# Optimization experiments

Hardware: AMD Instinct MI355X
Metric: run time of the kernel (lower is better)

Reference implementation:

```python
import jax, jax.numpy as jnp
import numpy as np

N_HEAD = 12

def setup_inputs() -> dict:
    key = jax.random.key(0)
    k1, k2, k3 = jax.random.split(key, 3)
    B, T, C = 8, 1024, 768
    x = jax.random.normal(k1, (B, T, C), dtype=jnp.float32)
    # Linear weights stored as [in, out] so y = x @ W + b (same math as torch Linear)
    w_attn = jax.random.normal(k2, (C, 3 * C), dtype=jnp.float32) * (1.0 / np.sqrt(C))
    b_attn = jnp.zeros((3 * C,), dtype=jnp.float32)
    w_proj = jax.random.normal(k3, (C, C), dtype=jnp.float32) * (1.0 / np.sqrt(C))
    b_proj = jnp.zeros((C,), dtype=jnp.float32)
    return {"x": x, "w_attn": w_attn, "b_attn": b_attn, "w_proj": w_proj, "b_proj": b_proj}

def reference(x, w_attn, b_attn, w_proj, b_proj):
    B, T, C = x.shape
    H = N_HEAD
    D = C // H
    qkv = x @ w_attn + b_attn                        # [B,T,3C]
    q, k, v = jnp.split(qkv, 3, axis=-1)             # each [B,T,C]
    q = q.reshape(B, T, H, D).transpose(0, 2, 1, 3)  # [B,H,T,D]
    k = k.reshape(B, T, H, D).transpose(0, 2, 1, 3)
    v = v.reshape(B, T, H, D).transpose(0, 2, 1, 3)
    scale = 1.0 / jnp.sqrt(jnp.asarray(D, dtype=x.dtype))
    att = jnp.einsum('bhqd,bhkd->bhqk', q, k) * scale  # [B,H,T,T]
    causal = jnp.tril(jnp.ones((T, T), dtype=bool))    # [T,T]
    att = jnp.where(causal[None, None], att, jnp.asarray(-jnp.inf, dtype=att.dtype))
    att = jax.nn.softmax(att, axis=-1)
    out = jnp.einsum('bhqk,bhkd->bhqd', att, v)        # [B,H,T,D]
    out = out.transpose(0, 2, 1, 3).reshape(B, T, C)
    return out @ w_proj + b_proj
```

## Files before the change

kernel.cpp:

```cpp
#include <hip/hip_runtime.h>
#include <hip/hip_bf16.h>
#include <cmath>

#define B_ 8
#define T_ 1024
#define C_ 768
#define H_ 12
#define D_ 64
#define N3C 2304
#define M_ 8192

typedef __bf16 bf16x4 __attribute__((ext_vector_type(4)));
typedef __bf16 bf16x8 __attribute__((ext_vector_type(8)));
typedef float  f32x4  __attribute__((ext_vector_type(4)));

typedef const __attribute__((address_space(1))) void* gptr_t;
typedef __attribute__((address_space(3))) void* lptr_t;

#define LOG2E 1.44269504088896f

__device__ __forceinline__ bf16x8 cvt_bf16x8(const float4& a, const float4& b) {
    bf16x8 r;
    r[0] = (__bf16)a.x; r[1] = (__bf16)a.y; r[2] = (__bf16)a.z; r[3] = (__bf16)a.w;
    r[4] = (__bf16)b.x; r[5] = (__bf16)b.y; r[6] = (__bf16)b.z; r[7] = (__bf16)b.w;
    return r;
}

__global__ __launch_bounds__(256) void prepass(const float* __restrict__ x,
                                               __bf16* __restrict__ xb,
                                               const float* __restrict__ wa,
                                               __bf16* __restrict__ wat,
                                               const float* __restrict__ wp,
                                               __bf16* __restrict__ wpt) {
    __shared__ float tile[32][33];
    const int bx = blockIdx.x, tid = threadIdx.x;
    if (bx < 3072) {
        int i = (bx * 256 + tid) * 8;
        float4 a = *(const float4*)&x[i];
        float4 b = *(const float4*)&x[i + 4];
        *(bf16x8*)&xb[i] = cvt_bf16x8(a, b);
        return;
    }
    const float* w;
    __bf16* wt;
    int K, N, n0, k0;
    if (bx < 4800) {
        int bb = bx - 3072;
        w = wa; wt = wat; K = 768; N = 2304;
        n0 = (bb % 72) * 32; k0 = (bb / 72) * 32;
    } else {
        int bb = bx - 4800;
        w = wp; wt = wpt; K = 768; N = 768;
        n0 = (bb % 24) * 32; k0 = (bb / 24) * 32;
    }
    int tx = tid & 31, ty = tid >> 5;
#pragma unroll
    for (int i = 0; i < 4; i++)
        tile[ty + i * 8][tx] = w[(size_t)(k0 + ty + i * 8) * N + n0 + tx];
    __syncthreads();
#pragma unroll
    for (int i = 0; i < 4; i++)
        wt[(size_t)(n0 + ty + i * 8) * K + k0 + tx] = (__bf16)tile[tx][ty + i * 8];
}

__global__ __launch_bounds__(512, 2) void qkv_gemm_mfma(const __bf16* __restrict__ A,
                                                        const __bf16* __restrict__ Bt,
                                                        const float* __restrict__ bias,
                                                        __bf16* __restrict__ qb,
                                                        __bf16* __restrict__ kb,
                                                        __bf16* __restrict__ vbt) {
    __shared__ __bf16 smem[73728];
    __bf16* Abuf = smem;
    __bf16* Bbuf = smem + 49152;
    const int tid = threadIdx.x;
    const int wave = tid >> 6, lane = tid & 63;
    const int lane15 = lane & 15, quad = lane >> 4;
    const int swz = (blockIdx.x & 7) * 72 + (blockIdx.x >> 3);
    const int n0 = (swz % 18) * 128;
    const int m0 = (swz / 18) * 256;
    const int wm = (wave >> 1) * 64, wn = (wave & 1) * 64;
    f32x4 acc[4][4] = {};

#define ISSUE_A2(KC, R0)                                                            \
    {                                                                               \
        const int k0s = (KC) * 64;                                                  \
        __bf16* Ad = Abuf + ((KC) % 3) * 16384;                                     \
        _Pragma("unroll")                                                           \
        for (int r = (R0); r < (R0) + 2; ++r) {                                     \
            int p = r * 512 + tid;                                                  \
            int row = p >> 3, csw = p & 7;                                          \
            __builtin_amdgcn_global_load_lds(                                       \
                (gptr_t)(A + (size_t)(m0 + row) * 768 + k0s + (csw ^ (row & 7)) * 8), \
                (lptr_t)(Ad + (r * 512 + wave * 64) * 8), 16, 0, 0);                \
        }                                                                           \
    }

#define ISSUE_B1(KC, R0)                                                            \
    {                                                                               \
        const int k0s = (KC) * 64;                                                  \
        __bf16* Bd = Bbuf + ((KC) % 3) * 8192;                                      \
        int p = (R0) * 512 + tid;                                                   \
        int row = p >> 3, csw = p & 7;                                              \
        __builtin_amdgcn_global_load_lds(                                           \
            (gptr_t)(Bt + (size_t)(n0 + row) * 768 + k0s + (csw ^ (row & 7)) * 8),  \
            (lptr_t)(Bd + ((R0) * 512 + wave * 64) * 8), 16, 0, 0);                 \
    }

#define BAR() asm volatile("s_barrier" ::: "memory")

    ISSUE_A2(0, 0); ISSUE_A2(0, 2); ISSUE_B1(0, 0); ISSUE_B1(0, 1);
    ISSUE_A2(1, 0); ISSUE_A2(1, 2); ISSUE_B1(1, 0); ISSUE_B1(1, 1);

    for (int kc = 0; kc < 12; ++kc) {
        if (kc < 11) { asm volatile("s_waitcnt vmcnt(6)" ::: "memory"); }
        else         { asm volatile("s_waitcnt vmcnt(0)" ::: "memory"); }
        BAR();
        const __bf16* Ac = Abuf + (kc % 3) * 16384;
        const __bf16* Bc = Bbuf + (kc % 3) * 8192;
        const bool pf = (kc + 2 < 12);

        bf16x8 af[4], bfr[2];
#pragma unroll
        for (int mt = 0; mt < 4; ++mt) {
            int m = wm + mt * 16 + lane15;
            af[mt] = *(const bf16x8*)(Ac + m * 64 + (quad ^ (m & 7)) * 8);
        }
#pragma unroll
        for (int nt = 0; nt < 2; ++nt) {
            int n = wn + nt * 16 + lane15;
            bfr[nt] = *(const bf16x8*)(Bc + n * 64 + (quad ^ (n & 7)) * 8);
        }
        if (pf) ISSUE_A2(kc + 2, 0);
        BAR();
        __builtin_amdgcn_s_setprio(1);
#pragma unroll
        for (int mt = 0; mt < 4; ++mt)
#pragma unroll
            for (int nt = 0; nt < 2; ++nt)
                acc[mt][nt] = __builtin_amdgcn_mfma_f32_16x16x32_bf16(af[mt], bfr[nt], acc[mt][nt], 0, 0, 0);
        __builtin_amdgcn_s_setprio(0);

#pragma unroll
        for (int nt = 0; nt < 2; ++nt) {
            int n = wn + (2 + nt) * 16 + lane15;
            bfr[nt] = *(const bf16x8*)(Bc + n * 64 + (quad ^ (n & 7)) * 8);
        }
        if (pf) ISSUE_A2(kc + 2, 2);
        BAR();
        __builtin_amdgcn_s_setprio(1);
#pragma unroll
        for (int mt = 0; mt < 4; ++mt)
#pragma unroll
            for (int nt = 0; nt < 2; ++nt)
                acc[mt][2 + nt] = __builtin_amdgcn_mfma_f32_16x16x32_bf16(af[mt], bfr[nt], acc[mt][2 + nt], 0, 0, 0);
        __builtin_amdgcn_s_setprio(0);

#pragma unroll
        for (int mt = 0; mt < 4; ++mt) {
            int m = wm + mt * 16 + lane15;
            af[mt] = *(const bf16x8*)(Ac + m * 64 + ((4 + quad) ^ (m & 7)) * 8);
        }
#pragma unroll
        for (int nt = 0; nt < 2; ++nt) {
            int n = wn + nt * 16 + lane15;
            bfr[nt] = *(const bf16x8*)(Bc + n * 64 + ((4 + quad) ^ (n & 7)) * 8);
        }
        if (pf) ISSUE_B1(kc + 2, 0);
        BAR();
        __builtin_amdgcn_s_setprio(1);
#pragma unroll
        for (int mt = 0; mt < 4; ++mt)
#pragma unroll
            for (int nt = 0; nt < 2; ++nt)
                acc[mt][nt] = __builtin_amdgcn_mfma_f32_16x16x32_bf16(af[mt], bfr[nt], acc[mt][nt], 0, 0, 0);
        __builtin_amdgcn_s_setprio(0);

#pragma unroll
        for (int nt = 0; nt < 2; ++nt) {
            int n = wn + (2 + nt) * 16 + lane15;
            bfr[nt] = *(const bf16x8*)(Bc + n * 64 + ((4 + quad) ^ (n & 7)) * 8);
        }
        if (pf) ISSUE_B1(kc + 2, 1);
        BAR();
        __builtin_amdgcn_s_setprio(1);
#pragma unroll
        for (int mt = 0; mt < 4; ++mt)
#pragma unroll
            for (int nt = 0; nt < 2; ++nt)
                acc[mt][2 + nt] = __builtin_amdgcn_mfma_f32_16x16x32_bf16(af[mt], bfr[nt], acc[mt][2 + nt], 0, 0, 0);
        __builtin_amdgcn_s_setprio(0);
    }

    if (n0 < 1536) {
        const bool isq = (n0 < 768);
        const float sc = isq ? (0.125f * LOG2E) : 1.0f;
#pragma unroll
        for (int nt = 0; nt < 4; ++nt) {
            int n = n0 + wn + nt * 16 + lane15;
            int rem = isq ? n : (n - 768);
            int h = rem >> 6;
            int d = n & 63;
            float bv = bias[n];
            __bf16* dst = isq ? qb : kb;
#pragma unroll
            for (int mt = 0; mt < 4; ++mt) {
#pragma unroll
                for (int reg = 0; reg < 4; ++reg) {
                    int mr = m0 + wm + mt * 16 + quad * 4 + reg;
                    int bb = mr >> 10, t = mr & 1023;
                    dst[(((size_t)bb * H_ + h) * T_ + t) * D_ + d] =
                        (__bf16)((acc[mt][nt][reg] + bv) * sc);
                }
            }
        }
    } else {
        __syncthreads();
        __bf16* vls = smem;
#pragma unroll
        for (int nt = 0; nt < 4; ++nt) {
            int nl = wn + nt * 16 + lane15;
            float bv = bias[n0 + nl];
#pragma unroll
            for (int mt = 0; mt < 4; ++mt)
#pragma unroll
                for (int reg = 0; reg < 4; ++reg)
                    vls[nl * 264 + wm + mt * 16 + quad * 4 + reg] =
                        (__bf16)(acc[mt][nt][reg] + bv);
        }
        __syncthreads();
        int nl = tid >> 2;
        int t0 = (tid & 3) * 64;
        int n = n0 + nl;
        int h = (n - 1536) >> 6;
        int d = n & 63;
        int bb = m0 >> 10, tg = (m0 & 1023) + t0;
        __bf16* dst = vbt + (((size_t)bb * H_ + h) * D_ + d) * T_ + tg;
        const __bf16* srcl = vls + nl * 264 + t0;
#pragma unroll
        for (int c = 0; c < 8; ++c) {
            bf16x8 v;
#pragma unroll
            for (int i = 0; i < 8; ++i) {
                int s = c * 8 + i;
                v[i] = srcl[(s & 3) * 16 + (s >> 2)];
            }
            *(bf16x8*)(dst + c * 8) = v;
        }
    }
#undef ISSUE_A2
#undef ISSUE_B1
#undef BAR
}

__global__ __launch_bounds__(256) void proj_gemm_mfma(const __bf16* __restrict__ A,
                                                      const __bf16* __restrict__ Bt,
                                                      const float* __restrict__ bias,
                                                      float* __restrict__ out) {
    __shared__ __bf16 As[128 * 64];
    __shared__ __bf16 Bs[64 * 64];
    const int tid = threadIdx.x;
    const int wave = tid >> 6, lane = tid & 63;
    const int lane15 = lane & 15, quad = lane >> 4;
    const int bid = blockIdx.x;
    const int m0 = ((bid & 7) * 8 + ((bid >> 3) & 7)) * 128;
    const int n0 = (bid >> 6) * 64;
    const int wm = wave * 32;
    f32x4 acc[2][4] = {};

#define PSTAGE(KC)                                                                  \
    {                                                                               \
        const int k0s = (KC) * 64;                                                  \
        _Pragma("unroll")                                                           \
        for (int r = 0; r < 4; ++r) {                                               \
            int p = r * 256 + tid;                                                  \
            int mrow = p >> 3, csw = p & 7;                                         \
            int ksrc = (csw ^ (mrow & 7)) * 8;                                      \
            __builtin_amdgcn_global_load_lds(                                       \
                (gptr_t)(A + (size_t)(m0 + mrow) * 768 + k0s + ksrc),               \
                (lptr_t)(&As[0] + (r * 256 + wave * 64) * 8), 16, 0, 0);            \
        }                                                                           \
        _Pragma("unroll")                                                           \
        for (int r = 0; r < 2; ++r) {                                               \
            int p = r * 256 + tid;                                                  \
            int nrow = p >> 3, csw = p & 7;                                         \
            int ksrc = (csw ^ (nrow & 7)) * 8;                                      \
            __builtin_amdgcn_global_load_lds(                                       \
                (gptr_t)(Bt + (size_t)(n0 + nrow) * 768 + k0s + ksrc),              \
                (lptr_t)(&Bs[0] + (r * 256 + wave * 64) * 8), 16, 0, 0);            \
        }                                                                           \
    }

    for (int kc = 0; kc < 12; ++kc) {
        PSTAGE(kc);
        __syncthreads();
#pragma unroll
        for (int ks = 0; ks < 2; ++ks) {
            bf16x8 af[2], bf[4];
#pragma unroll
            for (int mt = 0; mt < 2; ++mt) {
                int m = wm + mt * 16 + lane15;
                int csw = (ks * 4 + quad) ^ (m & 7);
                af[mt] = *(const bf16x8*)(&As[0] + m * 64 + csw * 8);
            }
#pragma unroll
            for (int nt = 0; nt < 4; ++nt) {
                int n = nt * 16 + lane15;
                int csw = (ks * 4 + quad) ^ (n & 7);
                bf[nt] = *(const bf16x8*)(&Bs[0] + n * 64 + csw * 8);
            }
#pragma unroll
            for (int mt = 0; mt < 2; ++mt)
#pragma unroll
                for (int nt = 0; nt < 4; ++nt)
                    acc[mt][nt] = __builtin_amdgcn_mfma_f32_16x16x32_bf16(af[mt], bf[nt], acc[mt][nt], 0, 0, 0);
        }
        __syncthreads();
    }

#pragma unroll
    for (int nt = 0; nt < 4; ++nt) {
        int n = n0 + nt * 16 + lane15;
        float bv = bias[n];
#pragma unroll
        for (int mt = 0; mt < 2; ++mt) {
#pragma unroll
            for (int reg = 0; reg < 4; ++reg) {
                int mr = m0 + wm + mt * 16 + quad * 4 + reg;
                out[(size_t)mr * C_ + n] = acc[mt][nt][reg] + bv;
            }
        }
    }
#undef PSTAGE
}

__global__ __launch_bounds__(256) void attn_mfma(const __bf16* __restrict__ qb,
                                                 const __bf16* __restrict__ kb,
                                                 const __bf16* __restrict__ vbt,
                                                 __bf16* __restrict__ ao) {
    __shared__ __bf16 Ks[2][64 * 64];
    __shared__ __bf16 Vts[2][64 * 64];
    __shared__ __bf16 Ps[4 * 16 * 72];

    const int tid = threadIdx.x;
    const int wave = tid >> 6, lane = tid & 63;
    const int lane15 = lane & 15, quad = lane >> 4;
    const int bh = blockIdx.x;
    const int y = blockIdx.y;
    const int qtA = 15 - y;
    const int qtB = y;
    const int kuA = qtA + 1;
    const int UT = 17;
    const int b = bh / H_, h = bh % H_;

    const __bf16* Kb = kb + (size_t)bh * T_ * D_;
    const __bf16* Vb = vbt + (size_t)bh * D_ * T_;
    __bf16* Pw = Ps + wave * 16 * 72;

    bf16x8 qfA[2], qfB[2];
    {
        const __bf16* qrA = qb + ((size_t)bh * T_ + qtA * 64 + wave * 16 + lane15) * D_ + quad * 8;
        qfA[0] = *(const bf16x8*)qrA;
        qfA[1] = *(const bf16x8*)(qrA + 32);
        const __bf16* qrB = qb + ((size_t)bh * T_ + qtB * 64 + wave * 16 + lane15) * D_ + quad * 8;
        qfB[0] = *(const bf16x8*)qrB;
        qfB[1] = *(const bf16x8*)(qrB + 32);
    }

    f32x4 o[4] = {};
    float lsum[4] = {0.f, 0.f, 0.f, 0.f};

#define ASTAGE(K0S, BUF)                                                           \
    {                                                                              \
        const int k0s = (K0S);                                                     \
        _Pragma("unroll")                                                          \
        for (int r = 0; r < 2; ++r) {                                              \
            int p = r * 256 + tid;                                                 \
            int row = p >> 3, c = p & 7;                                           \
            int cs = (c ^ (row & 7)) * 8;                                          \
            __builtin_amdgcn_global_load_lds(                                      \
                (gptr_t)(Kb + (size_t)(k0s + row) * D_ + cs),                      \
                (lptr_t)(&Ks[BUF][0] + (r * 256 + wave * 64) * 8), 16, 0, 0);      \
            __builtin_amdgcn_global_load_lds(                                      \
                (gptr_t)(Vb + (size_t)row * T_ + k0s + cs),                        \
                (lptr_t)(&Vts[BUF][0] + (r * 256 + wave * 64) * 8), 16, 0, 0);     \
        }                                                                          \
    }

    ASTAGE(0, 0);

    for (int u = 0; u < UT; ++u) {
        const int seg = (u >= kuA) ? 1 : 0;
        const int qt = seg ? qtB : qtA;
        const int k0 = (seg ? (u - kuA) : u) * 64;
        __syncthreads();
        if (u + 1 < UT) {
            const int un = u + 1;
            const int k0n = (un < kuA) ? un * 64 : (un - kuA) * 64;
            ASTAGE(k0n, un & 1);
        }
        const __bf16* Kc = &Ks[u & 1][0];
        const __bf16* Vc = &Vts[u & 1][0];

        const bf16x8 q0r = seg ? qfB[0] : qfA[0];
        const bf16x8 q1r = seg ? qfB[1] : qfA[1];

        f32x4 s[4];
        __builtin_amdgcn_s_setprio(1);
#pragma unroll
        for (int kt = 0; kt < 4; ++kt) {
            int row = kt * 16 + lane15;
            bf16x8 kf0 = *(const bf16x8*)(Kc + row * 64 + ((quad) ^ (row & 7)) * 8);
            bf16x8 kf1 = *(const bf16x8*)(Kc + row * 64 + ((4 + quad) ^ (row & 7)) * 8);
            f32x4 t = {};
            t = __builtin_amdgcn_mfma_f32_16x16x32_bf16(q0r, kf0, t, 0, 0, 0);
            t = __builtin_amdgcn_mfma_f32_16x16x32_bf16(q1r, kf1, t, 0, 0, 0);
            s[kt] = t;
        }
        __builtin_amdgcn_s_setprio(0);

        const bool diag = (k0 == qt * 64);
#pragma unroll
        for (int r = 0; r < 4; ++r) {
            bf16x4 pk;
#pragma unroll
            for (int kt = 0; kt < 4; ++kt) {
                int col = k0 + kt * 16 + lane15;
                float p = __builtin_amdgcn_exp2f(s[kt][r]);
                if (diag) {
                    int qrow = qt * 64 + wave * 16 + quad * 4 + r;
                    if (col > qrow) p = 0.f;
                }
                lsum[r] += p;
                pk[kt] = (__bf16)p;
            }
            *(bf16x4*)(Pw + (quad * 4 + r) * 72 + lane15 * 4) = pk;
        }

        bf16x8 vf[4][2];
#pragma unroll
        for (int dt = 0; dt < 4; ++dt) {
            int row = dt * 16 + lane15;
#pragma unroll
            for (int half = 0; half < 2; ++half)
                vf[dt][half] = *(const bf16x8*)(Vc + row * 64 + ((half * 4 + quad) ^ (row & 7)) * 8);
        }
        __builtin_amdgcn_s_setprio(1);
#pragma unroll
        for (int half = 0; half < 2; ++half) {
            bf16x8 pf = *(const bf16x8*)(Pw + lane15 * 72 + half * 32 + quad * 8);
#pragma unroll
            for (int dt = 0; dt < 4; ++dt)
                o[dt] = __builtin_amdgcn_mfma_f32_16x16x32_bf16(pf, vf[dt][half], o[dt], 0, 0, 0);
        }
        __builtin_amdgcn_s_setprio(0);

        if (u == kuA - 1 || u == UT - 1) {
            const int q0 = qt * 64;
            float inv[4];
#pragma unroll
            for (int r = 0; r < 4; ++r) {
                float ls = lsum[r];
                ls += __shfl_xor(ls, 1);
                ls += __shfl_xor(ls, 2);
                ls += __shfl_xor(ls, 4);
                ls += __shfl_xor(ls, 8);
                inv[r] = 1.0f / ls;
                lsum[r] = 0.f;
            }
#pragma unroll
            for (int dt = 0; dt < 4; ++dt) {
#pragma unroll
                for (int r = 0; r < 4; ++r) {
                    int t = q0 + wave * 16 + quad * 4 + r;
                    ao[((size_t)(b * T_ + t)) * C_ + h * 64 + dt * 16 + lane15] =
                        (__bf16)(o[dt][r] * inv[r]);
                }
                o[dt] = f32x4{};
            }
        }
    }
#undef ASTAGE
}

extern "C" void kernel_launch(void* const* d_in, const int* in_sizes, int n_in,
                              void* d_out, int out_size, void* d_ws, size_t ws_size,
                              hipStream_t stream) {
    const float* x = (const float*)d_in[0];
    const float* w_attn = (const float*)d_in[1];
    const float* b_attn = (const float*)d_in[2];
    const float* w_proj = (const float*)d_in[3];
    const float* b_proj = (const float*)d_in[4];
    float* out = (float*)d_out;

    __bf16* xb = (__bf16*)d_ws;
    __bf16* wat = xb + (size_t)M_ * C_;
    __bf16* wpt = wat + (size_t)N3C * C_;
    __bf16* qb = wpt + (size_t)C_ * C_;
    __bf16* kb = qb + (size_t)96 * T_ * D_;
    __bf16* vbt = kb + (size_t)96 * T_ * D_;
    __bf16* ao = vbt + (size_t)96 * T_ * D_;

    prepass<<<5376, 256, 0, stream>>>(x, xb, w_attn, wat, w_proj, wpt);
    qkv_gemm_mfma<<<576, 512, 0, stream>>>(xb, wat, b_attn, qb, kb, vbt);
    attn_mfma<<<dim3(96, 8), 256, 0, stream>>>(qb, kb, vbt, ao);
    proj_gemm_mfma<<<768, 256, 0, stream>>>(ao, wpt, b_proj, out);
}
```

Measured before the change: 168.9 us.

## Share K/V tiles between paired query tiles in causal attention loop

Each block processes two query tiles (qtA = 15-y and qtB = y). The loop used to stream K/V for tile A and then reload the K/V prefix again for tile B, 17 iterations in all. It now loops only over A's key range and reuses each loaded K/V tile and its register fragments for B while u <= qtB. This removes the duplicate global-to-LDS traffic and the extra barriers for B's keys, at the cost of more registers for a second accumulator set, which may reduce occupancy.

```diff
diff --git a/kernel.cpp b/kernel.cpp
--- a/kernel.cpp
+++ b/kernel.cpp
@@ -349,7 +349,6 @@
     const int qtA = 15 - y;
     const int qtB = y;
     const int kuA = qtA + 1;
-    const int UT = 17;
     const int b = bh / H_, h = bh % H_;
 
     const __bf16* Kb = kb + (size_t)bh * T_ * D_;
@@ -366,8 +365,8 @@
         qfB[1] = *(const bf16x8*)(qrB + 32);
     }
 
-    f32x4 o[4] = {};
-    float lsum[4] = {0.f, 0.f, 0.f, 0.f};
+    f32x4 oA[4] = {}, oB[4] = {};
+    float lsA[4] = {0.f, 0.f, 0.f, 0.f}, lsB[4] = {0.f, 0.f, 0.f, 0.f};
 
 #define ASTAGE(K0S, BUF)                                                           \
     {                                                                              \
@@ -388,54 +387,21 @@
 
     ASTAGE(0, 0);
 
-    for (int u = 0; u < UT; ++u) {
-        const int seg = (u >= kuA) ? 1 : 0;
-        const int qt = seg ? qtB : qtA;
-        const int k0 = (seg ? (u - kuA) : u) * 64;
+    for (int u = 0; u < kuA; ++u) {
+        const int k0 = u * 64;
         __syncthreads();
-        if (u + 1 < UT) {
-            const int un = u + 1;
-            const int k0n = (un < kuA) ? un * 64 : (un - kuA) * 64;
-            ASTAGE(k0n, un & 1);
-        }
+        if (u + 1 < kuA) ASTAGE((u + 1) * 64, (u + 1) & 1);
         const __bf16* Kc = &Ks[u & 1][0];
         const __bf16* Vc = &Vts[u & 1][0];
-
-        const bf16x8 q0r = seg ? qfB[0] : qfA[0];
-        const bf16x8 q1r = seg ? qfB[1] : qfA[1];
-
-        f32x4 s[4];
-        __builtin_amdgcn_s_setprio(1);
+        const bool doB = (u <= qtB);
+
+        bf16x8 kf0[4], kf1[4];
 #pragma unroll
         for (int kt = 0; kt < 4; ++kt) {
             int row = kt * 16 + lane15;
-            bf16x8 kf0 = *(const bf16x8*)(Kc + row * 64 + ((quad) ^ (row & 7)) * 8);
-            bf16x8 kf1 = *(const bf16x8*)(Kc + row * 64 + ((4 + quad) ^ (row & 7)) * 8);
-            f32x4 t = {};
-            t = __builtin_amdgcn_mfma_f32_16x16x32_bf16(q0r, kf0, t, 0, 0, 0);
-            t = __builtin_amdgcn_mfma_f32_16x16x32_bf16(q1r, kf1, t, 0, 0, 0);
-            s[kt] = t;
-        }
-        __builtin_amdgcn_s_setprio(0);
-
-        const bool diag = (k0 == qt * 64);
-#pragma unroll
-        for (int r = 0; r < 4; ++r) {
-            bf16x4 pk;
-#pragma unroll
-            for (int kt = 0; kt < 4; ++kt) {
-                int col = k0 + kt * 16 + lane15;
-                float p = __builtin_amdgcn_exp2f(s[kt][r]);
-                if (diag) {
-                    int qrow = qt * 64 + wave * 16 + quad * 4 + r;
-                    if (col > qrow) p = 0.f;
-                }
-                lsum[r] += p;
-                pk[kt] = (__bf16)p;
-            }
-            *(bf16x4*)(Pw + (quad * 4 + r) * 72 + lane15 * 4) = pk;
-        }
-
+            kf0[kt] = *(const bf16x8*)(Kc + row * 64 + ((quad) ^ (row & 7)) * 8);
+            kf1[kt] = *(const bf16x8*)(Kc + row * 64 + ((4 + quad) ^ (row & 7)) * 8);
+        }
         bf16x8 vf[4][2];
 #pragma unroll
         for (int dt = 0; dt < 4; ++dt) {
@@ -444,38 +410,126 @@
             for (int half = 0; half < 2; ++half)
                 vf[dt][half] = *(const bf16x8*)(Vc + row * 64 + ((half * 4 + quad) ^ (row & 7)) * 8);
         }
-        __builtin_amdgcn_s_setprio(1);
-#pragma unroll
-        for (int half = 0; half < 2; ++half) {
-            bf16x8 pf = *(const bf16x8*)(Pw + lane15 * 72 + half * 32 + quad * 8);
-#pragma unroll
-            for (int dt = 0; dt < 4; ++dt)
-                o[dt] = __builtin_amdgcn_mfma_f32_16x16x32_bf16(pf, vf[dt][half], o[dt], 0, 0, 0);
-        }
-        __builtin_amdgcn_s_setprio(0);
-
-        if (u == kuA - 1 || u == UT - 1) {
-            const int q0 = qt * 64;
-            float inv[4];
+
+        {
+            f32x4 s[4];
+            __builtin_amdgcn_s_setprio(1);
+#pragma unroll
+            for (int kt = 0; kt < 4; ++kt) {
+                f32x4 t = {};
+                t = __builtin_amdgcn_mfma_f32_16x16x32_bf16(qfA[0], kf0[kt], t, 0, 0, 0);
+                t = __builtin_amdgcn_mfma_f32_16x16x32_bf16(qfA[1], kf1[kt], t, 0, 0, 0);
+                s[kt] = t;
+            }
+            __builtin_amdgcn_s_setprio(0);
+            const bool diag = (u == qtA);
 #pragma unroll
             for (int r = 0; r < 4; ++r) {
-                float ls = lsum[r];
-                ls += __shfl_xor(ls, 1);
-                ls += __shfl_xor(ls, 2);
-                ls += __shfl_xor(ls, 4);
-                ls += __shfl_xor(ls, 8);
-                inv[r] = 1.0f / ls;
-                lsum[r] = 0.f;
-            }
-#pragma unroll
-            for (int dt = 0; dt < 4; ++dt) {
+                bf16x4 pk;
+#pragma unroll
+                for (int kt = 0; kt < 4; ++kt) {
+                    int col = k0 + kt * 16 + lane15;
+                    float p = __builtin_amdgcn_exp2f(s[kt][r]);
+                    if (diag) {
+                        int qrow = qtA * 64 + wave * 16 + quad * 4 + r;
+                        if (col > qrow) p = 0.f;
+                    }
+                    lsA[r] += p;
+                    pk[kt] = (__bf16)p;
+                }
+                *(bf16x4*)(Pw + (quad * 4 + r) * 72 + lane15 * 4) = pk;
+            }
+            __builtin_amdgcn_s_setprio(1);
+#pragma unroll
+            for (int half = 0; half < 2; ++half) {
+                bf16x8 pf = *(const bf16x8*)(Pw + lane15 * 72 + half * 32 + quad * 8);
+#pragma unroll
+                for (int dt = 0; dt < 4; ++dt)
+                    oA[dt] = __builtin_amdgcn_mfma_f32_16x16x32_bf16(pf, vf[dt][half], oA[dt], 0, 0, 0);
+            }
+            __builtin_amdgcn_s_setprio(0);
+        }
+
+        if (doB) {
+            f32x4 s[4];
+            __builtin_amdgcn_s_setprio(1);
+#pragma unroll
+            for (int kt = 0; kt < 4; ++kt) {
+                f32x4 t = {};
+                t = __builtin_amdgcn_mfma_f32_16x16x32_bf16(qfB[0], kf0[kt], t, 0, 0, 0);
+                t = __builtin_amdgcn_mfma_f32_16x16x32_bf16(qfB[1], kf1[kt], t, 0, 0, 0);
+                s[kt] = t;
+            }
+            __builtin_amdgcn_s_setprio(0);
+            const bool diag = (u == qtB);
+#pragma unroll
+            for (int r = 0; r < 4; ++r) {
+                bf16x4 pk;
+#pragma unroll
+                for (int kt = 0; kt < 4; ++kt) {
+                    int col = k0 + kt * 16 + lane15;
+                    float p = __builtin_amdgcn_exp2f(s[kt][r]);
+                    if (diag) {
+                        int qrow = qtB * 64 + wave * 16 + quad * 4 + r;
+                        if (col > qrow) p = 0.f;
+                    }
+                    lsB[r] += p;
+                    pk[kt] = (__bf16)p;
+                }
+                *(bf16x4*)(Pw + (quad * 4 + r) * 72 + lane15 * 4) = pk;
+            }
+            __builtin_amdgcn_s_setprio(1);
+#pragma unroll
+            for (int half = 0; half < 2; ++half) {
+                bf16x8 pf = *(const bf16x8*)(Pw + lane15 * 72 + half * 32 + quad * 8);
+#pragma unroll
+                for (int dt = 0; dt < 4; ++dt)
+                    oB[dt] = __builtin_amdgcn_mfma_f32_16x16x32_bf16(pf, vf[dt][half], oB[dt], 0, 0, 0);
+            }
+            __builtin_amdgcn_s_setprio(0);
+
+            if (u == qtB) {
+                float inv[4];
 #pragma unroll
                 for (int r = 0; r < 4; ++r) {
-                    int t = q0 + wave * 16 + quad * 4 + r;
-                    ao[((size_t)(b * T_ + t)) * C_ + h * 64 + dt * 16 + lane15] =
-                        (__bf16)(o[dt][r] * inv[r]);
+                    float ls = lsB[r];
+                    ls += __shfl_xor(ls, 1);
+                    ls += __shfl_xor(ls, 2);
+                    ls += __shfl_xor(ls, 4);
+                    ls += __shfl_xor(ls, 8);
+                    inv[r] = 1.0f / ls;
                 }
-                o[dt] = f32x4{};
+#pragma unroll
+                for (int dt = 0; dt < 4; ++dt) {
+#pragma unroll
+                    for (int r = 0; r < 4; ++r) {
+                        int t = qtB * 64 + wave * 16 + quad * 4 + r;
+                        ao[((size_t)(b * T_ + t)) * C_ + h * 64 + dt * 16 + lane15] =
+                            (__bf16)(oB[dt][r] * inv[r]);
+                    }
+                }
+            }
+        }
+    }
+
+    {
+        float inv[4];
+#pragma unroll
+        for (int r = 0; r < 4; ++r) {
+            float ls = lsA[r];
+            ls += __shfl_xor(ls, 1);
+            ls += __shfl_xor(ls, 2);
+            ls += __shfl_xor(ls, 4);
+            ls += __shfl_xor(ls, 8);
+            inv[r] = 1.0f / ls;
+        }
+#pragma unroll
+        for (int dt = 0; dt < 4; ++dt) {
+#pragma unroll
+            for (int r = 0; r < 4; ++r) {
+                int t = qtA * 64 + wave * 16 + quad * 4 + r;
+                ao[((size_t)(b * T_ + t)) * C_ + h * 64 + dt * 16 + lane15] =
+                    (__bf16)(oA[dt][r] * inv[r]);
             }
         }
     }
```

After: 177.3 us. 1.05x slower.

## Load K and V fragments directly from global memory in attention kernel

Applied to the files above, without the earlier changes.

Removes the double-buffered LDS staging of K and V tiles, the global_load_lds prefetch and the per-iteration __syncthreads. Each wave now reads its K and V MFMA fragments straight from global memory (relying on L1/L2), and the V loads are issued before QK^T. This drops the barrier and LDS traffic, but all four waves now re-read the same K/V data from cache instead of sharing one LDS copy, and there is no explicit prefetch to hide global latency.

```diff
diff --git a/kernel.cpp b/kernel.cpp
--- a/kernel.cpp
+++ b/kernel.cpp
@@ -337,8 +337,6 @@
                                                  const __bf16* __restrict__ kb,
                                                  const __bf16* __restrict__ vbt,
                                                  __bf16* __restrict__ ao) {
-    __shared__ __bf16 Ks[2][64 * 64];
-    __shared__ __bf16 Vts[2][64 * 64];
     __shared__ __bf16 Ps[4 * 16 * 72];
 
     const int tid = threadIdx.x;
@@ -369,48 +367,30 @@
     f32x4 o[4] = {};
     float lsum[4] = {0.f, 0.f, 0.f, 0.f};
 
-#define ASTAGE(K0S, BUF)                                                           \
-    {                                                                              \
-        const int k0s = (K0S);                                                     \
-        _Pragma("unroll")                                                          \
-        for (int r = 0; r < 2; ++r) {                                              \
-            int p = r * 256 + tid;                                                 \
-            int row = p >> 3, c = p & 7;                                           \
-            int cs = (c ^ (row & 7)) * 8;                                          \
-            __builtin_amdgcn_global_load_lds(                                      \
-                (gptr_t)(Kb + (size_t)(k0s + row) * D_ + cs),                      \
-                (lptr_t)(&Ks[BUF][0] + (r * 256 + wave * 64) * 8), 16, 0, 0);      \
-            __builtin_amdgcn_global_load_lds(                                      \
-                (gptr_t)(Vb + (size_t)row * T_ + k0s + cs),                        \
-                (lptr_t)(&Vts[BUF][0] + (r * 256 + wave * 64) * 8), 16, 0, 0);     \
-        }                                                                          \
-    }
-
-    ASTAGE(0, 0);
-
     for (int u = 0; u < UT; ++u) {
         const int seg = (u >= kuA) ? 1 : 0;
         const int qt = seg ? qtB : qtA;
         const int k0 = (seg ? (u - kuA) : u) * 64;
-        __syncthreads();
-        if (u + 1 < UT) {
-            const int un = u + 1;
-            const int k0n = (un < kuA) ? un * 64 : (un - kuA) * 64;
-            ASTAGE(k0n, un & 1);
-        }
-        const __bf16* Kc = &Ks[u & 1][0];
-        const __bf16* Vc = &Vts[u & 1][0];
 
         const bf16x8 q0r = seg ? qfB[0] : qfA[0];
         const bf16x8 q1r = seg ? qfB[1] : qfA[1];
 
+        bf16x8 vf[4][2];
+#pragma unroll
+        for (int dt = 0; dt < 4; ++dt) {
+            int row = dt * 16 + lane15;
+#pragma unroll
+            for (int half = 0; half < 2; ++half)
+                vf[dt][half] = *(const bf16x8*)(Vb + (size_t)row * T_ + k0 + (half * 4 + quad) * 8);
+        }
+
         f32x4 s[4];
         __builtin_amdgcn_s_setprio(1);
 #pragma unroll
         for (int kt = 0; kt < 4; ++kt) {
             int row = kt * 16 + lane15;
-            bf16x8 kf0 = *(const bf16x8*)(Kc + row * 64 + ((quad) ^ (row & 7)) * 8);
-            bf16x8 kf1 = *(const bf16x8*)(Kc + row * 64 + ((4 + quad) ^ (row & 7)) * 8);
+            bf16x8 kf0 = *(const bf16x8*)(Kb + (size_t)(k0 + row) * D_ + quad * 8);
+            bf16x8 kf1 = *(const bf16x8*)(Kb + (size_t)(k0 + row) * D_ + 32 + quad * 8);
             f32x4 t = {};
             t = __builtin_amdgcn_mfma_f32_16x16x32_bf16(q0r, kf0, t, 0, 0, 0);
             t = __builtin_amdgcn_mfma_f32_16x16x32_bf16(q1r, kf1, t, 0, 0, 0);
@@ -436,14 +416,6 @@
             *(bf16x4*)(Pw + (quad * 4 + r) * 72 + lane15 * 4) = pk;
         }
 
-        bf16x8 vf[4][2];
-#pragma unroll
-        for (int dt = 0; dt < 4; ++dt) {
-            int row = dt * 16 + lane15;
-#pragma unroll
-            for (int half = 0; half < 2; ++half)
-                vf[dt][half] = *(const bf16x8*)(Vc + row * 64 + ((half * 4 + quad) ^ (row & 7)) * 8);
-        }
         __builtin_amdgcn_s_setprio(1);
 #pragma unroll
         for (int half = 0; half < 2; ++half) {
@@ -479,7 +451,6 @@
             }
         }
     }
-#undef ASTAGE
 }
 
 extern "C" void kernel_launch(void* const* d_in, const int* in_sizes, int n_in,
```

Result: slower. 242.9 us (+43.8%).
